# Optimization experiments

Measured on AMD Instinct MI355X. Metric: run time of the kernel, lower is better.

## Reference

```python
import jax, jax.numpy as jnp
import numpy as np

EPS = 1e-4

def softmax_kernel(data, projection_matrix, is_query):
    # data: [b,h,n,d]; projection_matrix: [m,d]
    d = data.shape[-1]
    m = projection_matrix.shape[0]
    data_normalizer = d ** -0.25
    ratio = m ** -0.5
    # [b,h,n,m]
    data_dash = jnp.einsum('bhnd,md->bhnm', data_normalizer * data, projection_matrix)
    diag_data = jnp.sum(data ** 2, axis=-1, keepdims=True) * 0.5 * data_normalizer ** 2  # [b,h,n,1]
    if is_query:
        stab = jnp.max(data_dash, axis=-1, keepdims=True)
    else:
        stab = jnp.max(data_dash)
    return ratio * (jnp.exp(data_dash - diag_data - stab) + EPS)

def linear_attention(q, k, v):
    # q,k: [b,h,n,m]; v: [b,h,n,e]
    L = k.shape[-2]
    D_inv = 1.0 / jnp.einsum('bhnm,bhm->bhn', q, jnp.mean(k, axis=-2))  # [b,h,n]
    context = jnp.einsum('bhnm,bhne->bhme', k / float(L), v)            # [b,h,m,e]
    out = jnp.einsum('bhnm,bhme->bhne', D_inv[..., None] * q, context)  # [b,h,n,e]
    return out

def setup_inputs() -> dict:
    key = jax.random.key(0)
    k1, k2, k3, k4 = jax.random.split(key, 4)
    b, h, n, d = 4, 8, 4096, 64
    m = 266  # int(d * log(d))
    q = jax.random.normal(k1, (b, h, n, d), dtype=jnp.float32)
    k = jax.random.normal(k2, (b, h, n, d), dtype=jnp.float32)
    v = jax.random.normal(k3, (b, h, n, d), dtype=jnp.float32)
    projection_matrix = jax.random.normal(k4, (m, d), dtype=jnp.float32)
    return {"q": q, "k": k, "v": v, "projection_matrix": projection_matrix}

def reference(q, k, v, projection_matrix):
    qp = softmax_kernel(q, projection_matrix, is_query=True)
    kp = softmax_kernel(k, projection_matrix, is_query=False)
    return linear_attention(qp, kp, v)
```

## Files before the change

### kernel.cpp

```cpp
#include <hip/hip_runtime.h>
#include <cmath>


namespace {
constexpr float NORM       = 0.35355339059327379f;
constexpr float DIAG_SCALE = 0.0625f;
constexpr float EPSV       = 1e-4f;
constexpr float INV_L      = 1.0f / 4096.0f;

constexpr size_t OFF_PT  = 0;
constexpr size_t OFF_U   = OFF_PT + (size_t)64 * 272;
constexpr size_t OFF_u   = OFF_U + (size_t)32 * 272 * 64;
constexpr size_t OFF_SV  = OFF_u + (size_t)32 * 272;
constexpr size_t OFF_SC  = OFF_SV + (size_t)32 * 64;
constexpr size_t OFF_SK  = OFF_SC + (size_t)32 * 64;
constexpr size_t OFF_S   = OFF_SK + 32;
constexpr size_t OFF_CTX = OFF_S + 4;
constexpr size_t WS_FLOATS = OFF_CTX + (size_t)32 * 272 * 68;
}

__device__ __forceinline__ unsigned fenc(float f) {
  unsigned u = __float_as_uint(f);
  return (u & 0x80000000u) ? ~u : (u | 0x80000000u);
}
__device__ __forceinline__ float fdec(unsigned u) {
  return (u & 0x80000000u) ? __uint_as_float(u ^ 0x80000000u) : __uint_as_float(~u);
}

__device__ __forceinline__ void glds4(const float* g, float* l) {
  __builtin_amdgcn_global_load_lds((const __attribute__((address_space(1))) void*)g,
                                   (__attribute__((address_space(3))) void*)l, 4, 0, 0);
}
__device__ __forceinline__ void glds16(const float* g, float* l) {
  __builtin_amdgcn_global_load_lds((const __attribute__((address_space(1))) void*)g,
                                   (__attribute__((address_space(3))) void*)l, 16, 0, 0);
}

__global__ __launch_bounds__(256) void setup_kernel(const float* __restrict__ P,
                                                    float* __restrict__ ws) {
  const int t = threadIdx.x;
  const int elem = blockIdx.x * 256 + t;
  const int td = elem / 272, mm = elem % 272;
  ws[OFF_PT + (size_t)td * 272 + mm] = (mm < 266) ? NORM * P[mm * 64 + td] : 0.0f;
  if (blockIdx.x == 0 && t == 0) ((unsigned*)(ws + OFF_S))[0] = 0x007FFFFFu;
}

#define KQ_ROW(A1R, SQ, K4, P0, P1, P2, P3)                                     \
  {                                                                             \
    SQ = fmaf((K4).x, (K4).x, SQ);                                              \
    SQ = fmaf((K4).y, (K4).y, SQ);                                              \
    SQ = fmaf((K4).z, (K4).z, SQ);                                              \
    SQ = fmaf((K4).w, (K4).w, SQ);                                              \
    A1R[0] = fmaf((K4).x, (P0).x, A1R[0]);                                      \
    A1R[1] = fmaf((K4).x, (P0).y, A1R[1]);                                      \
    A1R[2] = fmaf((K4).x, (P0).z, A1R[2]);                                      \
    A1R[3] = fmaf((K4).x, (P0).w, A1R[3]);                                      \
    A1R[0] = fmaf((K4).y, (P1).x, A1R[0]);                                      \
    A1R[1] = fmaf((K4).y, (P1).y, A1R[1]);                                      \
    A1R[2] = fmaf((K4).y, (P1).z, A1R[2]);                                      \
    A1R[3] = fmaf((K4).y, (P1).w, A1R[3]);                                      \
    A1R[0] = fmaf((K4).z, (P2).x, A1R[0]);                                      \
    A1R[1] = fmaf((K4).z, (P2).y, A1R[1]);                                      \
    A1R[2] = fmaf((K4).z, (P2).z, A1R[2]);                                      \
    A1R[3] = fmaf((K4).z, (P2).w, A1R[3]);                                      \
    A1R[0] = fmaf((K4).w, (P3).x, A1R[0]);                                      \
    A1R[1] = fmaf((K4).w, (P3).y, A1R[1]);                                      \
    A1R[2] = fmaf((K4).w, (P3).z, A1R[2]);                                      \
    A1R[3] = fmaf((K4).w, (P3).w, A1R[3]);                                      \
  }

#define QC_ROW(AR, Q4, C0, C1, C2, C3)                                          \
  {                                                                             \
    AR[0] = fmaf((Q4).x, (C0).x, AR[0]);                                        \
    AR[1] = fmaf((Q4).x, (C0).y, AR[1]);                                        \
    AR[2] = fmaf((Q4).x, (C0).z, AR[2]);                                        \
    AR[3] = fmaf((Q4).x, (C0).w, AR[3]);                                        \
    AR[0] = fmaf((Q4).y, (C1).x, AR[0]);                                        \
    AR[1] = fmaf((Q4).y, (C1).y, AR[1]);                                        \
    AR[2] = fmaf((Q4).y, (C1).z, AR[2]);                                        \
    AR[3] = fmaf((Q4).y, (C1).w, AR[3]);                                        \
    AR[0] = fmaf((Q4).z, (C2).x, AR[0]);                                        \
    AR[1] = fmaf((Q4).z, (C2).y, AR[1]);                                        \
    AR[2] = fmaf((Q4).z, (C2).z, AR[2]);                                        \
    AR[3] = fmaf((Q4).z, (C2).w, AR[3]);                                        \
    AR[0] = fmaf((Q4).w, (C3).x, AR[0]);                                        \
    AR[1] = fmaf((Q4).w, (C3).y, AR[1]);                                        \
    AR[2] = fmaf((Q4).w, (C3).z, AR[2]);                                        \
    AR[3] = fmaf((Q4).w, (C3).w, AR[3]);                                        \
  }

__global__ __launch_bounds__(256) void pass_k_fused(const float* __restrict__ kg,
                                                    const float* __restrict__ vg,
                                                    float* __restrict__ ws) {
  __shared__ __align__(16) float pool[12544];
  __shared__ float redb[4];

  const int t = threadIdx.x;
  const int mb = blockIdx.x, bh = blockIdx.y, bz = blockIdx.z;
  const int lane = t & 63, wv = t >> 6;

  float* PTs = pool;
  float* kS  = pool + 4096;
  float* vS  = pool + 8448;

  const size_t base = ((size_t)bh * 4096 + (size_t)bz * 512) * 64;

  if (mb == 4) {
    const int m4 = t & 3, rg1 = t >> 2;
    const int eg = (t >> 2) & 15, rs = t >> 6;

    {
      const int td = t >> 2, m4i = t & 3;
      *(float4*)(PTs + td * 16 + m4i * 4) =
          *(const float4*)(ws + OFF_PT + (size_t)td * 272 + 256 + m4i * 4);
    }

    float acc2[4][4];
#pragma unroll
    for (int i = 0; i < 4; ++i) { acc2[i][0] = acc2[i][1] = acc2[i][2] = acc2[i][3] = 0.f; }
    float uacc[4] = {0, 0, 0, 0};
    float vsum[4] = {0, 0, 0, 0};
    float smax = -INFINITY;

    for (int sc = 0; sc < 8; ++sc) {
      const float* kgp = kg + base + (size_t)sc * 64 * 64;
      const float* vgp = vg + base + (size_t)sc * 64 * 64;
      __syncthreads();
      {
        const int r0 = wv * 16;
#pragma unroll
        for (int r = 0; r < 16; ++r) glds4(kgp + (r0 + r) * 64 + lane, kS + (r0 + r) * 68);
#pragma unroll
        for (int r4 = 0; r4 < 4; ++r4)
          glds16(vgp + (r0 + r4 * 4) * 64 + lane * 4, vS + (r0 + r4 * 4) * 64);
      }
      __syncthreads();
      float a1[4] = {0, 0, 0, 0};
      float sqt = 0.f;
#pragma unroll
      for (int tb = 0; tb < 16; ++tb) {
        const int td = tb * 4;
        const float4 kv4 = *(const float4*)(kS + rg1 * 68 + td);
        const float4 p0 = *(const float4*)(PTs + (td + 0) * 16 + m4 * 4);
        const float4 p1 = *(const float4*)(PTs + (td + 1) * 16 + m4 * 4);
        const float4 p2 = *(const float4*)(PTs + (td + 2) * 16 + m4 * 4);
        const float4 p3 = *(const float4*)(PTs + (td + 3) * 16 + m4 * 4);
        KQ_ROW(a1, sqt, kv4, p0, p1, p2, p3);
      }
      float vals[4];
      {
        const float dg = sqt * DIAG_SCALE;
#pragma unroll
        for (int j = 0; j < 4; ++j) {
          const int m = 256 + m4 * 4 + j;
          float e = 0.f;
          if (m < 266) {
            smax = fmaxf(smax, a1[j]);
            e = __expf(a1[j] - dg);
          }
          vals[j] = e;
        }
      }
      __syncthreads();
      {
        float4 st;
        st.x = vals[0]; st.y = vals[1]; st.z = vals[2]; st.w = vals[3];
        *(float4*)(kS + rg1 * 20 + m4 * 4) = st;
      }
      __syncthreads();
#pragma unroll 2
      for (int nn = 0; nn < 16; ++nn) {
        const int n = rs * 16 + nn;
        const float4 kk4 = *(const float4*)(kS + n * 20 + m4 * 4);
        const float4 vv4 = *(const float4*)(vS + n * 64 + eg * 4);
        const float kk[4] = {kk4.x, kk4.y, kk4.z, kk4.w};
        const float vv[4] = {vv4.x, vv4.y, vv4.z, vv4.w};
#pragma unroll
        for (int i = 0; i < 4; ++i)
#pragma unroll
          for (int j = 0; j < 4; ++j) acc2[i][j] = fmaf(kk[i], vv[j], acc2[i][j]);
        if (eg == 0) {
#pragma unroll
          for (int i = 0; i < 4; ++i) uacc[i] += kk[i];
        }
        if (m4 == 0) {
          vsum[0] += vv[0]; vsum[1] += vv[1]; vsum[2] += vv[2]; vsum[3] += vv[3];
        }
      }
    }
    {
      float* Ub = ws + OFF_U + ((size_t)bh * 272 + 256 + m4 * 4) * 64 + eg * 4;
#pragma unroll
      for (int i = 0; i < 4; ++i)
#pragma unroll
        for (int j = 0; j < 4; ++j) atomicAdd(Ub + (size_t)i * 64 + j, acc2[i][j]);
      if (eg == 0) {
#pragma unroll
        for (int i = 0; i < 4; ++i)
          atomicAdd(ws + OFF_u + (size_t)bh * 272 + 256 + m4 * 4 + i, uacc[i]);
      }
      if (m4 == 0) {
#pragma unroll
        for (int j = 0; j < 4; ++j)
          atomicAdd(ws + OFF_SV + bh * 64 + eg * 4 + j, vsum[j]);
      }
    }
#pragma unroll
    for (int o = 32; o > 0; o >>= 1) smax = fmaxf(smax, __shfl_xor(smax, o));
    if (lane == 0) redb[wv] = smax;
    __syncthreads();
    if (t == 0) {
      const float m = fmaxf(fmaxf(redb[0], redb[1]), fmaxf(redb[2], redb[3]));
      atomicMax((unsigned*)(ws + OFF_S), fenc(m));
    }
    return;
  }

  const int mq = t & 15, rg = t >> 4;
  const int mo = t & 7, eo = (t >> 3) & 7;
  const int rs = t >> 6;

#pragma unroll
  for (int c = 0; c < 4; ++c) {
    const int f4 = c * 256 + t;
    const int td = f4 >> 4, mi = f4 & 15;
    *(float4*)(PTs + td * 64 + mi * 4) =
        *(const float4*)(ws + OFF_PT + (size_t)td * 272 + mb * 64 + mi * 4);
  }

  float acc2[8][8];
#pragma unroll
  for (int i = 0; i < 8; ++i)
#pragma unroll
    for (int j = 0; j < 8; ++j) acc2[i][j] = 0.f;
  float uacc[8] = {0, 0, 0, 0, 0, 0, 0, 0};
  float smax = -INFINITY;

  for (int sc = 0; sc < 8; ++sc) {
    const float* kgp = kg + base + (size_t)sc * 64 * 64;
    const float* vgp = vg + base + (size_t)sc * 64 * 64;
    __syncthreads();
    {
      const int r0 = wv * 16;
#pragma unroll
      for (int r = 0; r < 16; ++r) glds4(kgp + (r0 + r) * 64 + lane, kS + (r0 + r) * 68);
#pragma unroll
      for (int r4 = 0; r4 < 4; ++r4)
        glds16(vgp + (r0 + r4 * 4) * 64 + lane * 4, vS + (r0 + r4 * 4) * 64);
    }
    __syncthreads();

    float a1[4][4];
#pragma unroll
    for (int i = 0; i < 4; ++i) { a1[i][0] = a1[i][1] = a1[i][2] = a1[i][3] = 0.f; }
    float sq[4] = {0, 0, 0, 0};
#pragma unroll
    for (int tb = 0; tb < 16; ++tb) {
      const int td = tb * 4;
      const float4 kA = *(const float4*)(kS + (rg * 4 + 0) * 68 + td);
      const float4 kB = *(const float4*)(kS + (rg * 4 + 1) * 68 + td);
      const float4 kC = *(const float4*)(kS + (rg * 4 + 2) * 68 + td);
      const float4 kD = *(const float4*)(kS + (rg * 4 + 3) * 68 + td);
      const float4 p0 = *(const float4*)(PTs + (td + 0) * 64 + mq * 4);
      const float4 p1 = *(const float4*)(PTs + (td + 1) * 64 + mq * 4);
      const float4 p2 = *(const float4*)(PTs + (td + 2) * 64 + mq * 4);
      const float4 p3 = *(const float4*)(PTs + (td + 3) * 64 + mq * 4);
      KQ_ROW(a1[0], sq[0], kA, p0, p1, p2, p3);
      KQ_ROW(a1[1], sq[1], kB, p0, p1, p2, p3);
      KQ_ROW(a1[2], sq[2], kC, p0, p1, p2, p3);
      KQ_ROW(a1[3], sq[3], kD, p0, p1, p2, p3);
    }
#pragma unroll
    for (int i = 0; i < 4; ++i) {
      const float dg = sq[i] * DIAG_SCALE;
      smax = fmaxf(smax, fmaxf(fmaxf(a1[i][0], a1[i][1]), fmaxf(a1[i][2], a1[i][3])));
      a1[i][0] = __expf(a1[i][0] - dg);
      a1[i][1] = __expf(a1[i][1] - dg);
      a1[i][2] = __expf(a1[i][2] - dg);
      a1[i][3] = __expf(a1[i][3] - dg);
    }
    __syncthreads();
#pragma unroll
    for (int i = 0; i < 4; ++i) {
      float4 st;
      st.x = a1[i][0]; st.y = a1[i][1]; st.z = a1[i][2]; st.w = a1[i][3];
      *(float4*)(kS + (rg * 4 + i) * 68 + mq * 4) = st;
    }
    __syncthreads();
#pragma unroll 2
    for (int nn = 0; nn < 16; ++nn) {
      const int n = rs * 16 + nn;
      const float4 ka = *(const float4*)(kS + n * 68 + mo * 8);
      const float4 kb = *(const float4*)(kS + n * 68 + mo * 8 + 4);
      const float4 va = *(const float4*)(vS + n * 64 + eo * 8);
      const float4 vb = *(const float4*)(vS + n * 64 + eo * 8 + 4);
      const float kk[8] = {ka.x, ka.y, ka.z, ka.w, kb.x, kb.y, kb.z, kb.w};
      const float vv[8] = {va.x, va.y, va.z, va.w, vb.x, vb.y, vb.z, vb.w};
#pragma unroll
      for (int i = 0; i < 8; ++i)
#pragma unroll
        for (int j = 0; j < 8; ++j) acc2[i][j] = fmaf(kk[i], vv[j], acc2[i][j]);
      if (eo == 0) {
#pragma unroll
        for (int i = 0; i < 8; ++i) uacc[i] += kk[i];
      }
    }
  }

  __syncthreads();
  {
    float* A = kS;
    float* B = PTs;
    if (wv == 1) {
#pragma unroll
      for (int i = 0; i < 8; ++i)
#pragma unroll
        for (int j = 0; j < 8; ++j) A[(i * 8 + j) * 64 + lane] = acc2[i][j];
    }
    if (wv == 3) {
#pragma unroll
      for (int i = 0; i < 8; ++i)
#pragma unroll
        for (int j = 0; j < 8; ++j) B[(i * 8 + j) * 64 + lane] = acc2[i][j];
    }
    __syncthreads();
    if (wv == 0) {
#pragma unroll
      for (int i = 0; i < 8; ++i)
#pragma unroll
        for (int j = 0; j < 8; ++j) acc2[i][j] += A[(i * 8 + j) * 64 + lane];
    }
    if (wv == 2) {
#pragma unroll
      for (int i = 0; i < 8; ++i)
#pragma unroll
        for (int j = 0; j < 8; ++j) acc2[i][j] += B[(i * 8 + j) * 64 + lane];
    }
    __syncthreads();
    if (wv == 2) {
#pragma unroll
      for (int i = 0; i < 8; ++i)
#pragma unroll
        for (int j = 0; j < 8; ++j) A[(i * 8 + j) * 64 + lane] = acc2[i][j];
    }
    __syncthreads();
    if (wv == 0) {
#pragma unroll
      for (int i = 0; i < 8; ++i)
#pragma unroll
        for (int j = 0; j < 8; ++j) {
          acc2[i][j] += A[(i * 8 + j) * 64 + lane];
          A[(i * 8 + j) * 64 + lane] = acc2[i][j];
        }
    }
    __syncthreads();
    {
      const int l = t & 63, idxb = (t >> 6) * 16;
      float* Ub = ws + OFF_U + ((size_t)bh * 272 + mb * 64) * 64;
#pragma unroll
      for (int c = 0; c < 16; ++c) {
        const int idx = idxb + c;
        const int ml = (l & 7) * 8 + (idx >> 3);
        const int e  = (l >> 3) * 8 + (idx & 7);
        atomicAdd(Ub + (size_t)ml * 64 + e, A[idx * 64 + l]);
      }
    }
    if (eo == 0) {
#pragma unroll
      for (int i = 0; i < 8; ++i)
        atomicAdd(ws + OFF_u + (size_t)bh * 272 + mb * 64 + mo * 8 + i, uacc[i]);
    }
  }
#pragma unroll
  for (int o = 32; o > 0; o >>= 1) smax = fmaxf(smax, __shfl_xor(smax, o));
  if (lane == 0) redb[wv] = smax;
  __syncthreads();
  if (t == 0) {
    const float m = fmaxf(fmaxf(redb[0], redb[1]), fmaxf(redb[2], redb[3]));
    atomicMax((unsigned*)(ws + OFF_S), fenc(m));
  }
}

__global__ __launch_bounds__(256) void combine_kernel(float* __restrict__ ws) {
  __shared__ float red[256];
  const int t = threadIdx.x;
  const int bh = blockIdx.x;
  const float S = fdec(((unsigned*)(ws + OFF_S))[0]);
  const float es = __expf(-S);
  const int e = t & 63, mr = t >> 6;
  const float svv = ws[OFF_SV + bh * 64 + e];
  float scp = 0.f;
  for (int mm = mr; mm < 272; mm += 4) {
    float val = 0.f;
    if (mm < 266)
      val = (es * ws[OFF_U + ((size_t)bh * 272 + mm) * 64 + e] + EPSV * svv) * INV_L;
    ws[OFF_CTX + ((size_t)bh * 272 + mm) * 68 + e] = val;
    scp += val;
  }
  red[t] = scp;
  __syncthreads();
  if (t < 64) ws[OFF_SC + bh * 64 + t] = red[t] + red[t + 64] + red[t + 128] + red[t + 192];
  __syncthreads();
  float skp = 0.f;
  for (int mm = t; mm < 272; mm += 256) {
    float km = 0.f;
    if (mm < 266) km = es * ws[OFF_u + (size_t)bh * 272 + mm] * INV_L + EPSV;
    float* cx = ws + OFF_CTX + ((size_t)bh * 272 + mm) * 68;
    cx[64] = km; cx[65] = 0.f; cx[66] = 0.f; cx[67] = 0.f;
    skp += km;
  }
  red[t] = skp;
  __syncthreads();
  for (int s = 128; s > 0; s >>= 1) {
    if (t < s) red[t] += red[t + s];
    __syncthreads();
  }
  if (t == 0) ws[OFF_SK + bh] = red[0];
}

__global__ __launch_bounds__(256) void pass_q(const float* __restrict__ qg,
                                              float* __restrict__ outg,
                                              const float* __restrict__ ws) {
  __shared__ __align__(16) float uni[8832];
  __shared__ unsigned rmx[32];
  __shared__ float Bl[32];

  const int t = threadIdx.x;
  const int nt = blockIdx.x, bh = blockIdx.y;
  const int lane = t & 63, wv = t >> 6;
  const float* qgp = qg + ((size_t)bh * 4096 + (size_t)nt * 32) * 64;

  if (t < 32) rmx[t] = 0x007FFFFFu;

#pragma unroll
  for (int r = 0; r < 8; ++r)
    glds4(qgp + (wv * 8 + r) * 64 + lane, uni + (wv * 8 + r) * 68);
  {
    const int td = t >> 2, j4 = t & 3;
    *(float4*)(uni + 2176 + td * 16 + j4 * 4) =
        *(const float4*)(ws + OFF_PT + (size_t)td * 272 + 256 + j4 * 4);
  }
  __syncthreads();

  const int mq = t & 63;
  float a1[8][4];
  float sq[8] = {0, 0, 0, 0, 0, 0, 0, 0};
#pragma unroll
  for (int i = 0; i < 8; ++i) { a1[i][0] = a1[i][1] = a1[i][2] = a1[i][3] = 0.f; }
  {
    const float* ptm = ws + OFF_PT + mq * 4;
    float4 pfA0, pfA1, pfA2, pfA3, pfB0, pfB1, pfB2, pfB3;
    pfA0 = *(const float4*)(ptm + (size_t)0 * 272);
    pfA1 = *(const float4*)(ptm + (size_t)1 * 272);
    pfA2 = *(const float4*)(ptm + (size_t)2 * 272);
    pfA3 = *(const float4*)(ptm + (size_t)3 * 272);
    pfB0 = *(const float4*)(ptm + (size_t)4 * 272);
    pfB1 = *(const float4*)(ptm + (size_t)5 * 272);
    pfB2 = *(const float4*)(ptm + (size_t)6 * 272);
    pfB3 = *(const float4*)(ptm + (size_t)7 * 272);
#pragma unroll
    for (int tb = 0; tb < 16; tb += 2) {
      {
        const int td = tb * 4;
#pragma unroll
        for (int i = 0; i < 8; ++i) {
          const float4 q4 = *(const float4*)(uni + (wv * 8 + i) * 68 + td);
          KQ_ROW(a1[i], sq[i], q4, pfA0, pfA1, pfA2, pfA3);
        }
        if (tb < 14) {
          pfA0 = *(const float4*)(ptm + (size_t)(td + 8) * 272);
          pfA1 = *(const float4*)(ptm + (size_t)(td + 9) * 272);
          pfA2 = *(const float4*)(ptm + (size_t)(td + 10) * 272);
          pfA3 = *(const float4*)(ptm + (size_t)(td + 11) * 272);
        }
      }
      {
        const int td = tb * 4 + 4;
#pragma unroll
        for (int i = 0; i < 8; ++i) {
          const float4 q4 = *(const float4*)(uni + (wv * 8 + i) * 68 + td);
          KQ_ROW(a1[i], sq[i], q4, pfB0, pfB1, pfB2, pfB3);
        }
        if (tb < 14) {
          pfB0 = *(const float4*)(ptm + (size_t)(td + 8) * 272);
          pfB1 = *(const float4*)(ptm + (size_t)(td + 9) * 272);
          pfB2 = *(const float4*)(ptm + (size_t)(td + 10) * 272);
          pfB3 = *(const float4*)(ptm + (size_t)(td + 11) * 272);
        }
      }
    }
  }
  float at[2] = {0.f, 0.f};
  float sqt[2] = {0.f, 0.f};
  const int mtl = t & 15;
  const int mt = 256 + mtl;
  const int r2 = (t >> 4) * 2;
  {
    const float* pts = uni + 2176 + mtl;
#pragma unroll
    for (int tb = 0; tb < 16; ++tb) {
      const int td = tb * 4;
      const float4 qx4 = *(const float4*)(uni + r2 * 68 + td);
      const float4 qy4 = *(const float4*)(uni + (r2 + 1) * 68 + td);
      const float p0 = pts[(td + 0) * 16];
      const float p1 = pts[(td + 1) * 16];
      const float p2 = pts[(td + 2) * 16];
      const float p3 = pts[(td + 3) * 16];
      sqt[0] = fmaf(qx4.x, qx4.x, sqt[0]);
      sqt[0] = fmaf(qx4.y, qx4.y, sqt[0]);
      sqt[0] = fmaf(qx4.z, qx4.z, sqt[0]);
      sqt[0] = fmaf(qx4.w, qx4.w, sqt[0]);
      sqt[1] = fmaf(qy4.x, qy4.x, sqt[1]);
      sqt[1] = fmaf(qy4.y, qy4.y, sqt[1]);
      sqt[1] = fmaf(qy4.z, qy4.z, sqt[1]);
      sqt[1] = fmaf(qy4.w, qy4.w, sqt[1]);
      at[0] = fmaf(qx4.x, p0, at[0]);
      at[0] = fmaf(qx4.y, p1, at[0]);
      at[0] = fmaf(qx4.z, p2, at[0]);
      at[0] = fmaf(qx4.w, p3, at[0]);
      at[1] = fmaf(qy4.x, p0, at[1]);
      at[1] = fmaf(qy4.y, p1, at[1]);
      at[1] = fmaf(qy4.z, p2, at[1]);
      at[1] = fmaf(qy4.w, p3, at[1]);
    }
  }
  __syncthreads();

#pragma unroll
  for (int i = 0; i < 8; ++i) {
    float lm = fmaxf(fmaxf(a1[i][0], a1[i][1]), fmaxf(a1[i][2], a1[i][3]));
#pragma unroll
    for (int o = 32; o > 0; o >>= 1) lm = fmaxf(lm, __shfl_xor(lm, o));
    if (lane == i) atomicMax(&rmx[wv * 8 + i], fenc(lm));
  }
#pragma unroll
  for (int s = 0; s < 2; ++s) {
    float v = (mt < 266) ? at[s] : -INFINITY;
#pragma unroll
    for (int o = 8; o > 0; o >>= 1) v = fmaxf(v, __shfl_xor(v, o));
    if ((t & 15) == 0) atomicMax(&rmx[r2 + s], fenc(v));
  }
#pragma unroll
  for (int i = 0; i < 8; ++i) {
    const int row = wv * 8 + i;
    const float dg = sq[i] * DIAG_SCALE;
    float4 st;
    st.x = __expf(a1[i][0] - dg);
    st.y = __expf(a1[i][1] - dg);
    st.z = __expf(a1[i][2] - dg);
    st.w = __expf(a1[i][3] - dg);
    *(float4*)(uni + row * 276 + mq * 4) = st;
  }
#pragma unroll
  for (int s = 0; s < 2; ++s) {
    const int row = r2 + s;
    uni[row * 276 + mt] = (mt < 266) ? __expf(at[s] - sqt[s] * DIAG_SCALE) : 0.f;
  }
  __syncthreads();

  const int cq2 = t & 15, rg2 = (t >> 4) & 7, ms = t >> 7;
  const float* ctxg = ws + OFF_CTX + (size_t)bh * 272 * 68;
  const float* crow = ctxg + cq2 * 4;
  const int mb0 = ms * 136;
  float acc[4][4];
#pragma unroll
  for (int i = 0; i < 4; ++i) { acc[i][0] = acc[i][1] = acc[i][2] = acc[i][3] = 0.f; }
  float accB[4] = {0, 0, 0, 0};
  float4 c0, c1, c2, c3, n0, n1, n2, n3;
  float cb0 = 0, cb1 = 0, cb2 = 0, cb3 = 0, nb0 = 0, nb1 = 0, nb2 = 0, nb3 = 0;
  c0 = *(const float4*)(crow + (size_t)(mb0 + 0) * 68);
  c1 = *(const float4*)(crow + (size_t)(mb0 + 1) * 68);
  c2 = *(const float4*)(crow + (size_t)(mb0 + 2) * 68);
  c3 = *(const float4*)(crow + (size_t)(mb0 + 3) * 68);
  if (cq2 == 0) {
    cb0 = ctxg[(size_t)(mb0 + 0) * 68 + 64];
    cb1 = ctxg[(size_t)(mb0 + 1) * 68 + 64];
    cb2 = ctxg[(size_t)(mb0 + 2) * 68 + 64];
    cb3 = ctxg[(size_t)(mb0 + 3) * 68 + 64];
  }
  for (int mc = 0; mc < 34; ++mc) {
    const int mm = mb0 + mc * 4;
    if (mc < 33) {
      n0 = *(const float4*)(crow + (size_t)(mm + 4) * 68);
      n1 = *(const float4*)(crow + (size_t)(mm + 5) * 68);
      n2 = *(const float4*)(crow + (size_t)(mm + 6) * 68);
      n3 = *(const float4*)(crow + (size_t)(mm + 7) * 68);
      if (cq2 == 0) {
        nb0 = ctxg[(size_t)(mm + 4) * 68 + 64];
        nb1 = ctxg[(size_t)(mm + 5) * 68 + 64];
        nb2 = ctxg[(size_t)(mm + 6) * 68 + 64];
        nb3 = ctxg[(size_t)(mm + 7) * 68 + 64];
      }
    }
    const float4 q0 = *(const float4*)(uni + (rg2 * 4 + 0) * 276 + mm);
    const float4 q1 = *(const float4*)(uni + (rg2 * 4 + 1) * 276 + mm);
    const float4 q2 = *(const float4*)(uni + (rg2 * 4 + 2) * 276 + mm);
    const float4 q3 = *(const float4*)(uni + (rg2 * 4 + 3) * 276 + mm);
    QC_ROW(acc[0], q0, c0, c1, c2, c3);
    QC_ROW(acc[1], q1, c0, c1, c2, c3);
    QC_ROW(acc[2], q2, c0, c1, c2, c3);
    QC_ROW(acc[3], q3, c0, c1, c2, c3);
    if (cq2 == 0) {
      accB[0] = fmaf(q0.x, cb0, accB[0]);
      accB[0] = fmaf(q0.y, cb1, accB[0]);
      accB[0] = fmaf(q0.z, cb2, accB[0]);
      accB[0] = fmaf(q0.w, cb3, accB[0]);
      accB[1] = fmaf(q1.x, cb0, accB[1]);
      accB[1] = fmaf(q1.y, cb1, accB[1]);
      accB[1] = fmaf(q1.z, cb2, accB[1]);
      accB[1] = fmaf(q1.w, cb3, accB[1]);
      accB[2] = fmaf(q2.x, cb0, accB[2]);
      accB[2] = fmaf(q2.y, cb1, accB[2]);
      accB[2] = fmaf(q2.z, cb2, accB[2]);
      accB[2] = fmaf(q2.w, cb3, accB[2]);
      accB[3] = fmaf(q3.x, cb0, accB[3]);
      accB[3] = fmaf(q3.y, cb1, accB[3]);
      accB[3] = fmaf(q3.z, cb2, accB[3]);
      accB[3] = fmaf(q3.w, cb3, accB[3]);
    }
    if (mc < 33) {
      c0 = n0; c1 = n1; c2 = n2; c3 = n3;
      cb0 = nb0; cb1 = nb1; cb2 = nb2; cb3 = nb3;
    }
  }

  __syncthreads();
  if (ms == 1) {
    const int p = t - 128;
#pragma unroll
    for (int i = 0; i < 4; ++i)
#pragma unroll
      for (int j = 0; j < 4; ++j) uni[(i * 4 + j) * 128 + p] = acc[i][j];
    if (cq2 == 0) {
#pragma unroll
      for (int i = 0; i < 4; ++i) uni[2048 + rg2 * 4 + i] = accB[i];
    }
  }
  __syncthreads();
  if (ms == 0) {
#pragma unroll
    for (int i = 0; i < 4; ++i)
#pragma unroll
      for (int j = 0; j < 4; ++j) acc[i][j] += uni[(i * 4 + j) * 128 + t];
    if (cq2 == 0) {
#pragma unroll
      for (int i = 0; i < 4; ++i) Bl[rg2 * 4 + i] = accB[i] + uni[2048 + rg2 * 4 + i];
    }
  }
  __syncthreads();

  if (ms == 0) {
    const float4 sc4 = *(const float4*)(ws + OFF_SC + bh * 64 + cq2 * 4);
    const float skv = ws[OFF_SK + bh];
    float* op = outg + ((size_t)bh * 4096 + (size_t)nt * 32) * 64;
#pragma unroll
    for (int i = 0; i < 4; ++i) {
      const int row = rg2 * 4 + i;
      const float rm = fdec(rmx[row]);
      const float tt = EPSV * __expf(rm);
      const float inv = 1.0f / (Bl[row] + tt * skv);
      float4 o;
      o.x = (acc[i][0] + tt * sc4.x) * inv;
      o.y = (acc[i][1] + tt * sc4.y) * inv;
      o.z = (acc[i][2] + tt * sc4.z) * inv;
      o.w = (acc[i][3] + tt * sc4.w) * inv;
      *(float4*)(op + row * 64 + cq2 * 4) = o;
    }
  }
}

extern "C" void kernel_launch(void* const* d_in, const int* in_sizes, int n_in,
                              void* d_out, int out_size, void* d_ws, size_t ws_size,
                              hipStream_t stream) {
  (void)in_sizes; (void)n_in; (void)out_size; (void)ws_size;
  const float* q = (const float*)d_in[0];
  const float* k = (const float*)d_in[1];
  const float* v = (const float*)d_in[2];
  const float* P = (const float*)d_in[3];
  float* out = (float*)d_out;
  float* ws = (float*)d_ws;

  hipMemsetAsync((void*)(ws + OFF_U), 0, (OFF_CTX - OFF_U) * sizeof(float), stream);
  setup_kernel<<<68, 256, 0, stream>>>(P, ws);
  pass_k_fused<<<dim3(5, 32, 8), 256, 0, stream>>>(k, v, ws);
  combine_kernel<<<32, 256, 0, stream>>>(ws);
  pass_q<<<dim3(128, 32), 256, 0, stream>>>(q, out, ws);
}
```

Measured before the change: 569.2 us.

## Precompute row squared norms once per tile and halve K-pass block count

Squared-norm (diag) terms were computed redundantly by every thread inside the projection loops. They are now computed once per row via a cooperative LDS reduction with shuffles and stored in shared memory. The K pass now launches half as many z-blocks, each covering 1024 rows instead of 512, which halves the atomic flushes of partial U results. The final U reduction also goes through a transposed padded LDS buffer so the atomics are row-contiguous, and the pass_q row stride changes from 276 to 272. The costs are an extra barrier per tile and less parallelism in the K pass.

```diff
diff --git a/kernel.cpp b/kernel.cpp
--- a/kernel.cpp
+++ b/kernel.cpp
@@ -45,12 +45,8 @@
   if (blockIdx.x == 0 && t == 0) ((unsigned*)(ws + OFF_S))[0] = 0x007FFFFFu;
 }
 
-#define KQ_ROW(A1R, SQ, K4, P0, P1, P2, P3)                                     \
+#define KQ_ROW(A1R, K4, P0, P1, P2, P3)                                         \
   {                                                                             \
-    SQ = fmaf((K4).x, (K4).x, SQ);                                              \
-    SQ = fmaf((K4).y, (K4).y, SQ);                                              \
-    SQ = fmaf((K4).z, (K4).z, SQ);                                              \
-    SQ = fmaf((K4).w, (K4).w, SQ);                                              \
     A1R[0] = fmaf((K4).x, (P0).x, A1R[0]);                                      \
     A1R[1] = fmaf((K4).x, (P0).y, A1R[1]);                                      \
     A1R[2] = fmaf((K4).x, (P0).z, A1R[2]);                                      \
@@ -93,6 +89,7 @@
                                                     const float* __restrict__ vg,
                                                     float* __restrict__ ws) {
   __shared__ __align__(16) float pool[12544];
+  __shared__ float diagS[64];
   __shared__ float redb[4];
 
   const int t = threadIdx.x;
@@ -103,7 +100,7 @@
   float* kS  = pool + 4096;
   float* vS  = pool + 8448;
 
-  const size_t base = ((size_t)bh * 4096 + (size_t)bz * 512) * 64;
+  const size_t base = ((size_t)bh * 4096 + (size_t)bz * 1024) * 64;
 
   if (mb == 4) {
     const int m4 = t & 3, rg1 = t >> 2;
@@ -122,7 +119,7 @@
     float vsum[4] = {0, 0, 0, 0};
     float smax = -INFINITY;
 
-    for (int sc = 0; sc < 8; ++sc) {
+    for (int sc = 0; sc < 16; ++sc) {
       const float* kgp = kg + base + (size_t)sc * 64 * 64;
       const float* vgp = vg + base + (size_t)sc * 64 * 64;
       __syncthreads();
@@ -135,8 +132,26 @@
           glds16(vgp + (r0 + r4 * 4) * 64 + lane * 4, vS + (r0 + r4 * 4) * 64);
       }
       __syncthreads();
+      {
+        const int dr = t >> 2, dq = t & 3;
+        const float4 s0 = *(const float4*)(kS + dr * 68 + dq * 16);
+        const float4 s1 = *(const float4*)(kS + dr * 68 + dq * 16 + 4);
+        const float4 s2 = *(const float4*)(kS + dr * 68 + dq * 16 + 8);
+        const float4 s3 = *(const float4*)(kS + dr * 68 + dq * 16 + 12);
+        float s = s0.x * s0.x;
+        s = fmaf(s0.y, s0.y, s); s = fmaf(s0.z, s0.z, s); s = fmaf(s0.w, s0.w, s);
+        s = fmaf(s1.x, s1.x, s); s = fmaf(s1.y, s1.y, s); s = fmaf(s1.z, s1.z, s);
+        s = fmaf(s1.w, s1.w, s);
+        s = fmaf(s2.x, s2.x, s); s = fmaf(s2.y, s2.y, s); s = fmaf(s2.z, s2.z, s);
+        s = fmaf(s2.w, s2.w, s);
+        s = fmaf(s3.x, s3.x, s); s = fmaf(s3.y, s3.y, s); s = fmaf(s3.z, s3.z, s);
+        s = fmaf(s3.w, s3.w, s);
+        s += __shfl_xor(s, 1);
+        s += __shfl_xor(s, 2);
+        if (dq == 0) diagS[dr] = s * DIAG_SCALE;
+      }
+      __syncthreads();
       float a1[4] = {0, 0, 0, 0};
-      float sqt = 0.f;
 #pragma unroll
       for (int tb = 0; tb < 16; ++tb) {
         const int td = tb * 4;
@@ -145,11 +160,11 @@
         const float4 p1 = *(const float4*)(PTs + (td + 1) * 16 + m4 * 4);
         const float4 p2 = *(const float4*)(PTs + (td + 2) * 16 + m4 * 4);
         const float4 p3 = *(const float4*)(PTs + (td + 3) * 16 + m4 * 4);
-        KQ_ROW(a1, sqt, kv4, p0, p1, p2, p3);
+        KQ_ROW(a1, kv4, p0, p1, p2, p3);
       }
       float vals[4];
       {
-        const float dg = sqt * DIAG_SCALE;
+        const float dg = diagS[rg1];
 #pragma unroll
         for (int j = 0; j < 4; ++j) {
           const int m = 256 + m4 * 4 + j;
@@ -236,7 +251,7 @@
   float uacc[8] = {0, 0, 0, 0, 0, 0, 0, 0};
   float smax = -INFINITY;
 
-  for (int sc = 0; sc < 8; ++sc) {
+  for (int sc = 0; sc < 16; ++sc) {
     const float* kgp = kg + base + (size_t)sc * 64 * 64;
     const float* vgp = vg + base + (size_t)sc * 64 * 64;
     __syncthreads();
@@ -249,11 +264,29 @@
         glds16(vgp + (r0 + r4 * 4) * 64 + lane * 4, vS + (r0 + r4 * 4) * 64);
     }
     __syncthreads();
+    {
+      const int dr = t >> 2, dq = t & 3;
+      const float4 s0 = *(const float4*)(kS + dr * 68 + dq * 16);
+      const float4 s1 = *(const float4*)(kS + dr * 68 + dq * 16 + 4);
+      const float4 s2 = *(const float4*)(kS + dr * 68 + dq * 16 + 8);
+      const float4 s3 = *(const float4*)(kS + dr * 68 + dq * 16 + 12);
+      float s = s0.x * s0.x;
+      s = fmaf(s0.y, s0.y, s); s = fmaf(s0.z, s0.z, s); s = fmaf(s0.w, s0.w, s);
+      s = fmaf(s1.x, s1.x, s); s = fmaf(s1.y, s1.y, s); s = fmaf(s1.z, s1.z, s);
+      s = fmaf(s1.w, s1.w, s);
+      s = fmaf(s2.x, s2.x, s); s = fmaf(s2.y, s2.y, s); s = fmaf(s2.z, s2.z, s);
+      s = fmaf(s2.w, s2.w, s);
+      s = fmaf(s3.x, s3.x, s); s = fmaf(s3.y, s3.y, s); s = fmaf(s3.z, s3.z, s);
+      s = fmaf(s3.w, s3.w, s);
+      s += __shfl_xor(s, 1);
+      s += __shfl_xor(s, 2);
+      if (dq == 0) diagS[dr] = s * DIAG_SCALE;
+    }
+    __syncthreads();
 
     float a1[4][4];
 #pragma unroll
     for (int i = 0; i < 4; ++i) { a1[i][0] = a1[i][1] = a1[i][2] = a1[i][3] = 0.f; }
-    float sq[4] = {0, 0, 0, 0};
 #pragma unroll
     for (int tb = 0; tb < 16; ++tb) {
       const int td = tb * 4;
@@ -265,14 +298,14 @@
       const float4 p1 = *(const float4*)(PTs + (td + 1) * 64 + mq * 4);
       const float4 p2 = *(const float4*)(PTs + (td + 2) * 64 + mq * 4);
       const float4 p3 = *(const float4*)(PTs + (td + 3) * 64 + mq * 4);
-      KQ_ROW(a1[0], sq[0], kA, p0, p1, p2, p3);
-      KQ_ROW(a1[1], sq[1], kB, p0, p1, p2, p3);
-      KQ_ROW(a1[2], sq[2], kC, p0, p1, p2, p3);
-      KQ_ROW(a1[3], sq[3], kD, p0, p1, p2, p3);
+      KQ_ROW(a1[0], kA, p0, p1, p2, p3);
+      KQ_ROW(a1[1], kB, p0, p1, p2, p3);
+      KQ_ROW(a1[2], kC, p0, p1, p2, p3);
+      KQ_ROW(a1[3], kD, p0, p1, p2, p3);
     }
 #pragma unroll
     for (int i = 0; i < 4; ++i) {
-      const float dg = sq[i] * DIAG_SCALE;
+      const float dg = diagS[rg * 4 + i];
       smax = fmaxf(smax, fmaxf(fmaxf(a1[i][0], a1[i][1]), fmaxf(a1[i][2], a1[i][3])));
       a1[i][0] = __expf(a1[i][0] - dg);
       a1[i][1] = __expf(a1[i][1] - dg);
@@ -309,60 +342,58 @@
 
   __syncthreads();
   {
-    float* A = kS;
-    float* B = PTs;
+    float* FA = vS;
+    float* FB = PTs;
     if (wv == 1) {
 #pragma unroll
       for (int i = 0; i < 8; ++i)
 #pragma unroll
-        for (int j = 0; j < 8; ++j) A[(i * 8 + j) * 64 + lane] = acc2[i][j];
+        for (int j = 0; j < 8; ++j) FA[(i * 8 + j) * 64 + lane] = acc2[i][j];
     }
     if (wv == 3) {
 #pragma unroll
       for (int i = 0; i < 8; ++i)
 #pragma unroll
-        for (int j = 0; j < 8; ++j) B[(i * 8 + j) * 64 + lane] = acc2[i][j];
+        for (int j = 0; j < 8; ++j) FB[(i * 8 + j) * 64 + lane] = acc2[i][j];
     }
     __syncthreads();
     if (wv == 0) {
 #pragma unroll
       for (int i = 0; i < 8; ++i)
 #pragma unroll
-        for (int j = 0; j < 8; ++j) acc2[i][j] += A[(i * 8 + j) * 64 + lane];
+        for (int j = 0; j < 8; ++j) acc2[i][j] += FA[(i * 8 + j) * 64 + lane];
     }
     if (wv == 2) {
 #pragma unroll
       for (int i = 0; i < 8; ++i)
 #pragma unroll
-        for (int j = 0; j < 8; ++j) acc2[i][j] += B[(i * 8 + j) * 64 + lane];
+        for (int j = 0; j < 8; ++j) acc2[i][j] += FB[(i * 8 + j) * 64 + lane];
     }
     __syncthreads();
     if (wv == 2) {
 #pragma unroll
       for (int i = 0; i < 8; ++i)
 #pragma unroll
-        for (int j = 0; j < 8; ++j) A[(i * 8 + j) * 64 + lane] = acc2[i][j];
+        for (int j = 0; j < 8; ++j) FA[(i * 8 + j) * 64 + lane] = acc2[i][j];
     }
     __syncthreads();
     if (wv == 0) {
+      const int mo8 = (lane & 7) * 8, eo8 = (lane >> 3) * 8;
 #pragma unroll
       for (int i = 0; i < 8; ++i)
 #pragma unroll
         for (int j = 0; j < 8; ++j) {
-          acc2[i][j] += A[(i * 8 + j) * 64 + lane];
-          A[(i * 8 + j) * 64 + lane] = acc2[i][j];
+          acc2[i][j] += FA[(i * 8 + j) * 64 + lane];
+          kS[(mo8 + i) * 65 + eo8 + j] = acc2[i][j];
         }
     }
     __syncthreads();
     {
-      const int l = t & 63, idxb = (t >> 6) * 16;
       float* Ub = ws + OFF_U + ((size_t)bh * 272 + mb * 64) * 64;
 #pragma unroll
-      for (int c = 0; c < 16; ++c) {
-        const int idx = idxb + c;
-        const int ml = (l & 7) * 8 + (idx >> 3);
-        const int e  = (l >> 3) * 8 + (idx & 7);
-        atomicAdd(Ub + (size_t)ml * 64 + e, A[idx * 64 + l]);
+      for (int r = 0; r < 16; ++r) {
+        const int row = wv * 16 + r;
+        atomicAdd(Ub + (size_t)row * 64 + lane, kS[row * 65 + lane]);
       }
     }
     if (eo == 0) {
@@ -421,7 +452,8 @@
 __global__ __launch_bounds__(256) void pass_q(const float* __restrict__ qg,
                                               float* __restrict__ outg,
                                               const float* __restrict__ ws) {
-  __shared__ __align__(16) float uni[8832];
+  __shared__ __align__(16) float uni[8704];
+  __shared__ float diagS[32];
   __shared__ unsigned rmx[32];
   __shared__ float Bl[32];
 
@@ -442,9 +474,23 @@
   }
   __syncthreads();
 
+  {
+    const int dr = t >> 3, d8 = t & 7;
+    const float4 s0 = *(const float4*)(uni + dr * 68 + d8 * 8);
+    const float4 s1 = *(const float4*)(uni + dr * 68 + d8 * 8 + 4);
+    float s = s0.x * s0.x;
+    s = fmaf(s0.y, s0.y, s); s = fmaf(s0.z, s0.z, s); s = fmaf(s0.w, s0.w, s);
+    s = fmaf(s1.x, s1.x, s); s = fmaf(s1.y, s1.y, s); s = fmaf(s1.z, s1.z, s);
+    s = fmaf(s1.w, s1.w, s);
+    s += __shfl_xor(s, 1);
+    s += __shfl_xor(s, 2);
+    s += __shfl_xor(s, 4);
+    if (d8 == 0) diagS[dr] = s * DIAG_SCALE;
+  }
+  __syncthreads();
+
   const int mq = t & 63;
   float a1[8][4];
-  float sq[8] = {0, 0, 0, 0, 0, 0, 0, 0};
 #pragma unroll
   for (int i = 0; i < 8; ++i) { a1[i][0] = a1[i][1] = a1[i][2] = a1[i][3] = 0.f; }
   {
@@ -465,7 +511,7 @@
 #pragma unroll
         for (int i = 0; i < 8; ++i) {
           const float4 q4 = *(const float4*)(uni + (wv * 8 + i) * 68 + td);
-          KQ_ROW(a1[i], sq[i], q4, pfA0, pfA1, pfA2, pfA3);
+          KQ_ROW(a1[i], q4, pfA0, pfA1, pfA2, pfA3);
         }
         if (tb < 14) {
           pfA0 = *(const float4*)(ptm + (size_t)(td + 8) * 272);
@@ -479,7 +525,7 @@
 #pragma unroll
         for (int i = 0; i < 8; ++i) {
           const float4 q4 = *(const float4*)(uni + (wv * 8 + i) * 68 + td);
-          KQ_ROW(a1[i], sq[i], q4, pfB0, pfB1, pfB2, pfB3);
+          KQ_ROW(a1[i], q4, pfB0, pfB1, pfB2, pfB3);
         }
         if (tb < 14) {
           pfB0 = *(const float4*)(ptm + (size_t)(td + 8) * 272);
@@ -491,7 +537,6 @@
     }
   }
   float at[2] = {0.f, 0.f};
-  float sqt[2] = {0.f, 0.f};
   const int mtl = t & 15;
   const int mt = 256 + mtl;
   const int r2 = (t >> 4) * 2;
@@ -506,14 +551,6 @@
       const float p1 = pts[(td + 1) * 16];
       const float p2 = pts[(td + 2) * 16];
       const float p3 = pts[(td + 3) * 16];
-      sqt[0] = fmaf(qx4.x, qx4.x, sqt[0]);
-      sqt[0] = fmaf(qx4.y, qx4.y, sqt[0]);
-      sqt[0] = fmaf(qx4.z, qx4.z, sqt[0]);
-      sqt[0] = fmaf(qx4.w, qx4.w, sqt[0]);
-      sqt[1] = fmaf(qy4.x, qy4.x, sqt[1]);
-      sqt[1] = fmaf(qy4.y, qy4.y, sqt[1]);
-      sqt[1] = fmaf(qy4.z, qy4.z, sqt[1]);
-      sqt[1] = fmaf(qy4.w, qy4.w, sqt[1]);
       at[0] = fmaf(qx4.x, p0, at[0]);
       at[0] = fmaf(qx4.y, p1, at[0]);
       at[0] = fmaf(qx4.z, p2, at[0]);
@@ -543,18 +580,18 @@
 #pragma unroll
   for (int i = 0; i < 8; ++i) {
     const int row = wv * 8 + i;
-    const float dg = sq[i] * DIAG_SCALE;
+    const float dg = diagS[row];
     float4 st;
     st.x = __expf(a1[i][0] - dg);
     st.y = __expf(a1[i][1] - dg);
     st.z = __expf(a1[i][2] - dg);
     st.w = __expf(a1[i][3] - dg);
-    *(float4*)(uni + row * 276 + mq * 4) = st;
+    *(float4*)(uni + row * 272 + mq * 4) = st;
   }
 #pragma unroll
   for (int s = 0; s < 2; ++s) {
     const int row = r2 + s;
-    uni[row * 276 + mt] = (mt < 266) ? __expf(at[s] - sqt[s] * DIAG_SCALE) : 0.f;
+    uni[row * 272 + mt] = (mt < 266) ? __expf(at[s] - diagS[row]) : 0.f;
   }
   __syncthreads();
 
@@ -592,10 +629,10 @@
         nb3 = ctxg[(size_t)(mm + 7) * 68 + 64];
       }
     }
-    const float4 q0 = *(const float4*)(uni + (rg2 * 4 + 0) * 276 + mm);
-    const float4 q1 = *(const float4*)(uni + (rg2 * 4 + 1) * 276 + mm);
-    const float4 q2 = *(const float4*)(uni + (rg2 * 4 + 2) * 276 + mm);
-    const float4 q3 = *(const float4*)(uni + (rg2 * 4 + 3) * 276 + mm);
+    const float4 q0 = *(const float4*)(uni + (rg2 * 4 + 0) * 272 + mm);
+    const float4 q1 = *(const float4*)(uni + (rg2 * 4 + 1) * 272 + mm);
+    const float4 q2 = *(const float4*)(uni + (rg2 * 4 + 2) * 272 + mm);
+    const float4 q3 = *(const float4*)(uni + (rg2 * 4 + 3) * 272 + mm);
     QC_ROW(acc[0], q0, c0, c1, c2, c3);
     QC_ROW(acc[1], q1, c0, c1, c2, c3);
     QC_ROW(acc[2], q2, c0, c1, c2, c3);
@@ -682,7 +719,7 @@
 
   hipMemsetAsync((void*)(ws + OFF_U), 0, (OFF_CTX - OFF_U) * sizeof(float), stream);
   setup_kernel<<<68, 256, 0, stream>>>(P, ws);
-  pass_k_fused<<<dim3(5, 32, 8), 256, 0, stream>>>(k, v, ws);
+  pass_k_fused<<<dim3(5, 32, 4), 256, 0, stream>>>(k, v, ws);
   combine_kernel<<<32, 256, 0, stream>>>(ws);
   pass_q<<<dim3(128, 32), 256, 0, stream>>>(q, out, ws);
 }
```

After: 488.3 us. 14.2% less time.
